# Optimization experiments

Measured on AMD Instinct MI355X. Metric: run time of the kernel, lower is better.

Reference implementation:

```python
import jax, jax.numpy as jnp
import numpy as np

D_MODEL = 256

def setup_inputs() -> dict:
    key = jax.random.key(0)
    k1, k2, k3, k4, k5, k6 = jax.random.split(key, 6)
    B, LQ, LK, D = 16, 2048, 2048, D_MODEL
    q = jax.random.normal(k1, (B, LQ, D), dtype=jnp.float32)
    k = jax.random.normal(k2, (B, LK, D), dtype=jnp.float32)
    tsp = jax.random.normal(k3, (B, LK, D), dtype=jnp.float32)
    # xavier_uniform for w_qk [D, D] (no bias)
    bound = float(np.sqrt(6.0 / (D + D)))
    w_qk = jax.random.uniform(k4, (D, D), minval=-bound, maxval=bound, dtype=jnp.float32)
    # linear1: default torch init kaiming-uniform-ish; any values fine for correctness baseline
    lim = float(1.0 / np.sqrt(D))
    w1 = jax.random.uniform(k5, (D, D), minval=-lim, maxval=lim, dtype=jnp.float32)
    b1 = jax.random.uniform(k6, (D,), minval=-lim, maxval=lim, dtype=jnp.float32)
    return {"q": q, "k": k, "tsp": tsp, "w_qk": w_qk, "w1": w1, "b1": b1}

def reference(q, k, tsp, w_qk, w1, b1):
    d_head = q.shape[-1]
    temperature = jnp.asarray(np.power(d_head, 0.5), dtype=q.dtype)
    residual = q
    # shared Q/K projection (torch Linear: x @ W^T)
    qp = jnp.einsum('bqd,ed->bqe', q, w_qk)            # [B, Lq, Dh]
    kp = jnp.einsum('bkd,ed->bke', k, w_qk)            # [B, Lk, Dh]
    logits = jnp.einsum('bqd,bkd->bqk', qp, kp) / temperature  # [B, Lq, Lk]
    attn = jax.nn.softmax(logits, axis=2)
    # sigmoid is monotonic: max(sigmoid(x)) == sigmoid(max(x))
    prob_fg = jax.nn.sigmoid(jnp.max(logits, axis=-1, keepdims=True))  # [B, Lq, 1]
    out = jnp.einsum('bqk,bkd->bqd', attn, tsp)        # [B, Lq, Dh]
    gated = (residual + out) * prob_fg
    return jnp.einsum('bqd,ed->bqe', gated, w1) + b1
```

## Files before the change

kernel.cpp:

```cpp
#include <hip/hip_runtime.h>
#include <hip/hip_bf16.h>

typedef __bf16 bf16;
typedef __bf16 bf16x8 __attribute__((ext_vector_type(8)));
typedef __bf16 bf16x4 __attribute__((ext_vector_type(4)));
typedef __bf16 bf16x2 __attribute__((ext_vector_type(2)));
typedef float f32x4 __attribute__((ext_vector_type(4)));

static __device__ __forceinline__ f32x4 mfma16(bf16x8 a, bf16x8 b, f32x4 c) {
    return __builtin_amdgcn_mfma_f32_16x16x32_bf16(a, b, c, 0, 0, 0);
}

static __device__ __forceinline__ void load16_to_lds(const void* g, void* l) {
    __builtin_amdgcn_global_load_lds(
        (const __attribute__((address_space(1))) unsigned int*)g,
        (__attribute__((address_space(3))) unsigned int*)l, 16, 0, 0);
}

#define LKV 2048
#define DM 256

template<bool IN_BF16, bool OUT_BF16, bool HAS_BIAS>
static __device__ __forceinline__ void gemm_body(char* smem,
                                                 const void* __restrict__ Xv,
                                                 const float* __restrict__ Wf,
                                                 const float* __restrict__ bias,
                                                 float scale, void* __restrict__ Y,
                                                 long rowbase) {
    bf16* Xl  = (bf16*)smem;
    char* WlB = smem + 33792;
    const int tid  = threadIdx.x;
    const int lane = tid & 63, wave = tid >> 6;
    const int hi = lane >> 4, lo = lane & 15;

    if (IN_BF16) {
        const bf16* Xb = (const bf16*)Xv;
#pragma unroll
        for (int i = 0; i < 8; ++i) {
            int idx = i * 256 + tid;
            int r = idx >> 5, c8 = (idx & 31) * 8;
            uint4 v = *(const uint4*)(Xb + (rowbase + r) * 256 + c8);
            *(uint4*)(Xl + r * 264 + c8) = v;
        }
    } else {
        const float* X = (const float*)Xv;
#pragma unroll
        for (int i = 0; i < 16; ++i) {
            int idx4 = i * 256 + tid;
            int e = idx4 * 4;
            int r = e >> 8, c = e & 255;
            float4 v = *(const float4*)(X + (rowbase + r) * 256 + c);
            bf16x4 o;
            o[0] = (bf16)v.x; o[1] = (bf16)v.y; o[2] = (bf16)v.z; o[3] = (bf16)v.w;
            *(bf16x4*)(Xl + r * 264 + c) = o;
        }
    }

    f32x4 acc[16];
    const f32x4 zero = {0.f, 0.f, 0.f, 0.f};
#pragma unroll
    for (int n = 0; n < 16; ++n) acc[n] = zero;

    for (int ks = 0; ks < 8; ++ks) {
        __syncthreads();
#pragma unroll
        for (int c = 0; c < 8; ++c) {
            int idx = c * 256 + tid;
            int e = idx >> 3, q4 = (idx & 7) * 4;
            float4 v = *(const float4*)(Wf + e * 256 + ks * 32 + q4);
            bf16x4 o;
            o[0] = (bf16)v.x; o[1] = (bf16)v.y; o[2] = (bf16)v.z; o[3] = (bf16)v.w;
            *(bf16x4*)(WlB + e * 80 + q4 * 2) = o;
        }
        __syncthreads();
        bf16x8 a = *(const bf16x8*)((const char*)Xl + (wave * 16 + lo) * 528 + ks * 64 + hi * 16);
#pragma unroll
        for (int n = 0; n < 16; ++n) {
            bf16x8 bfr = *(const bf16x8*)(WlB + (n * 16 + lo) * 80 + hi * 16);
            acc[n] = mfma16(a, bfr, acc[n]);
        }
    }

#pragma unroll
    for (int n = 0; n < 16; ++n) {
        int col = n * 16 + lo;
        float bv = HAS_BIAS ? bias[col] : 0.f;
#pragma unroll
        for (int r = 0; r < 4; ++r) {
            long row = rowbase + wave * 16 + hi * 4 + r;
            float v = acc[n][r] * scale + bv;
            if (OUT_BF16) ((bf16*)Y)[row * 256 + col] = (bf16)v;
            else          ((float*)Y)[row * 256 + col] = v;
        }
    }
}

__global__ __launch_bounds__(256) void prep_qk(const float* __restrict__ q,
                                               const float* __restrict__ k,
                                               const float* __restrict__ wqk,
                                               const float* __restrict__ tsp,
                                               bf16* __restrict__ qp,
                                               bf16* __restrict__ kp,
                                               bf16* __restrict__ tspF) {
    __shared__ __align__(16) char smem[54272];
    const int tid = threadIdx.x;
    int bid = (int)blockIdx.x;
    if (bid < 1024) {
        bool is_k = bid >= 512;
        gemm_body<false, true, false>(smem, is_k ? k : q, wqk, nullptr,
                                      is_k ? 1.0f : 0.0625f, is_k ? kp : qp,
                                      (long)(bid & 511) * 64);
        return;
    }
    int id = bid - 1024;
    const int b = id >> 7;
    const int kv0 = (id & 31) * 64, d0 = ((id >> 5) & 3) * 64;
    float (*tile)[65] = (float(*)[65])smem;
#pragma unroll
    for (int i = 0; i < 4; ++i) {
        int idx = i * 256 + tid;
        int kv = idx >> 4, c4 = (idx & 15) * 4;
        float4 v = *(const float4*)(tsp + ((long)(b * LKV + kv0 + kv)) * DM + d0 + c4);
        tile[kv][c4 + 0] = v.x; tile[kv][c4 + 1] = v.y;
        tile[kv][c4 + 2] = v.z; tile[kv][c4 + 3] = v.w;
    }
    __syncthreads();
    char* outb = (char*)tspF + ((long)b << 20);
#pragma unroll
    for (int i = 0; i < 2; ++i) {
        int w = i * 256 + tid;
        int ti = w >> 8;
        int dti = (w >> 6) & 3;
        int lane = w & 63;
        int hi = lane >> 4, lo = lane & 15;
        bf16x8 o;
#pragma unroll
        for (int j = 0; j < 8; ++j) o[j] = (bf16)tile[ti * 32 + hi * 8 + j][dti * 16 + lo];
        int t_abs = (kv0 >> 5) + ti;
        int dt_abs = (d0 >> 4) + dti;
        *(bf16x8*)(outb + (((t_abs * 16 + dt_abs) << 6) + lane) * 16) = o;
    }
}

__global__ __launch_bounds__(256) void gemm_out(const bf16* __restrict__ gated,
                                                const float* __restrict__ w1,
                                                const float* __restrict__ b1,
                                                float* __restrict__ out) {
    __shared__ __align__(16) char smem[54272];
    gemm_body<true, false, true>(smem, gated, w1, b1, 1.0f, out, (long)blockIdx.x * 64);
}

__global__ __launch_bounds__(256, 2) void flash6(const bf16* __restrict__ qp,
                                                 const bf16* __restrict__ kp,
                                                 const bf16* __restrict__ tspF,
                                                 const float* __restrict__ qorig,
                                                 bf16* __restrict__ gated) {
    __shared__ __align__(16) char kbuf[3][16384];
    const int tid  = threadIdx.x;
    const int lane = tid & 63, wave = tid >> 6;
    const int hi = lane >> 4, lo = lane & 15;

    int id  = (int)blockIdx.x;
    int bid = (id & 7) * 64 + (id >> 3);
    const int b  = bid >> 5;
    const int qb = bid & 31;
    const long qbase = (long)b * LKV + qb * 64;
    const char* kp_g  = (const char*)(kp + (long)b * LKV * DM);
    const char* tsp_f = (const char*)tspF + ((long)b << 20) + lane * 16;

    int kp_off[4];
#pragma unroll
    for (int j = 0; j < 4; ++j) {
        int kv = wave * 8 + j * 2 + (lane >> 5);
        kp_off[j] = kv * 512 + (((lane & 31) ^ (kv & 7)) << 4);
    }

    int bp_src[4];
#pragma unroll
    for (int k2 = 0; k2 < 4; ++k2)
        bp_src[k2] = ((((hi & 1) * 2 + (k2 >> 1)) << 4) + lo) << 2;

    bf16x8 aq[8];
    {
        const bf16* qrow = qp + (qbase + wave * 16 + lo) * DM;
#pragma unroll
        for (int ks = 0; ks < 8; ++ks) aq[ks] = *(const bf16x8*)(qrow + ks * 32 + hi * 8);
    }

    bf16x8 ones;
#pragma unroll
    for (int j = 0; j < 8; ++j) ones[j] = (bf16)1.0f;

    f32x4 o[16], o_l;
    const f32x4 zero = {0.f, 0.f, 0.f, 0.f};
#pragma unroll
    for (int n = 0; n < 16; ++n) o[n] = zero;
    o_l = zero;
    float m = -1e30f, tm = -1e30f;

    const int kswz = (lo & 7) << 4;

#pragma unroll
    for (int j = 0; j < 4; ++j)
        load16_to_lds(kp_g + kp_off[j],          &kbuf[0][wave * 4096 + j * 1024]);
#pragma unroll
    for (int j = 0; j < 4; ++j)
        load16_to_lds(kp_g + 16384 + kp_off[j],  &kbuf[1][wave * 4096 + j * 1024]);

    for (int t = 0; t < 64; ++t) {
        if (t == 0)       { asm volatile("s_waitcnt vmcnt(4)"  ::: "memory"); }
        else if (t == 63) { asm volatile("s_waitcnt vmcnt(16)" ::: "memory"); }
        else              { asm volatile("s_waitcnt vmcnt(20)" ::: "memory"); }
        __builtin_amdgcn_sched_barrier(0);
        __builtin_amdgcn_s_barrier();
        __builtin_amdgcn_sched_barrier(0);

        bf16x8 tt[16];
        {
            const char* tb = tsp_f + (long)t * 16384;
#pragma unroll
            for (int dt = 0; dt < 16; ++dt)
                tt[dt] = *(const bf16x8*)(tb + dt * 1024);
        }
        if (t < 62) {
            const int dslot = (t + 2) % 3;
            const char* src = kp_g + (long)(t + 2) * 16384;
#pragma unroll
            for (int j = 0; j < 4; ++j)
                load16_to_lds(src + kp_off[j], &kbuf[dslot][wave * 4096 + j * 1024]);
        }
        __builtin_amdgcn_sched_barrier(0);

        f32x4 s[2];
        const char* kb = kbuf[t % 3];
        __builtin_amdgcn_s_setprio(1);
#pragma unroll
        for (int n = 0; n < 2; ++n) {
            s[n] = zero;
            const char* rowp = kb + ((n * 16 + lo) << 9);
#pragma unroll
            for (int ks = 0; ks < 8; ++ks) {
                bf16x8 kk = *(const bf16x8*)(rowp + ((ks * 64 + hi * 16) ^ kswz));
                s[n] = mfma16(kk, aq[ks], s[n]);
            }
        }
        __builtin_amdgcn_s_setprio(0);

        float pm = fmaxf(fmaxf(fmaxf(s[0][0], s[0][1]), fmaxf(s[0][2], s[0][3])),
                         fmaxf(fmaxf(s[1][0], s[1][1]), fmaxf(s[1][2], s[1][3])));
        pm = fmaxf(pm, __shfl_xor(pm, 16));
        pm = fmaxf(pm, __shfl_xor(pm, 32));
        tm = fmaxf(tm, pm);
        if (__any(pm > m + 8.f)) {
            float nm = fmaxf(m, pm);
            float a = __expf(m - nm);
            m = nm;
            o_l *= a;
#pragma unroll
            for (int n = 0; n < 16; ++n) o[n] *= a;
        }
        int cvt[2][2];
#pragma unroll
        for (int n = 0; n < 2; ++n)
#pragma unroll
            for (int c = 0; c < 2; ++c) {
                bf16x2 pr;
                pr[0] = (bf16)__expf(s[n][2 * c]     - m);
                pr[1] = (bf16)__expf(s[n][2 * c + 1] - m);
                cvt[n][c] = __builtin_bit_cast(int, pr);
            }
        int pki[4];
#pragma unroll
        for (int k2 = 0; k2 < 4; ++k2) {
            int a0 = __builtin_amdgcn_ds_bpermute(bp_src[k2], cvt[0][k2 & 1]);
            int a1 = __builtin_amdgcn_ds_bpermute(bp_src[k2], cvt[1][k2 & 1]);
            pki[k2] = (hi < 2) ? a0 : a1;
        }
        int4 pii = make_int4(pki[0], pki[1], pki[2], pki[3]);
        bf16x8 pk = __builtin_bit_cast(bf16x8, pii);

        o_l = mfma16(ones, pk, o_l);
        __builtin_amdgcn_s_setprio(1);
#pragma unroll
        for (int dt = 0; dt < 16; ++dt)
            o[dt] = mfma16(tt[dt], pk, o[dt]);
        __builtin_amdgcn_s_setprio(0);
    }

    float prob = 1.f / (1.f + __expf(-tm));
    float invl = 1.f / o_l[0];
    long row = qbase + wave * 16 + lo;
#pragma unroll
    for (int dt = 0; dt < 16; ++dt) {
        int c0 = dt * 16 + hi * 4;
        float4 qv = *(const float4*)(qorig + row * 256 + c0);
        bf16x4 g;
        g[0] = (bf16)((qv.x + o[dt][0] * invl) * prob);
        g[1] = (bf16)((qv.y + o[dt][1] * invl) * prob);
        g[2] = (bf16)((qv.z + o[dt][2] * invl) * prob);
        g[3] = (bf16)((qv.w + o[dt][3] * invl) * prob);
        *(bf16x4*)(gated + row * 256 + c0) = g;
    }
}

extern "C" void kernel_launch(void* const* d_in, const int* in_sizes, int n_in,
                              void* d_out, int out_size, void* d_ws, size_t ws_size,
                              hipStream_t stream) {
    const float* q    = (const float*)d_in[0];
    const float* k    = (const float*)d_in[1];
    const float* tsp  = (const float*)d_in[2];
    const float* w_qk = (const float*)d_in[3];
    const float* w1   = (const float*)d_in[4];
    const float* b1   = (const float*)d_in[5];
    float* out = (float*)d_out;
    char* ws = (char*)d_ws;

    bf16* qp_b  = (bf16*)(ws + 0);
    bf16* kp_b  = (bf16*)(ws + 16777216);
    bf16* tspF  = (bf16*)(ws + 33554432);
    bf16* gated = (bf16*)(ws + 50331648);

    prep_qk<<<3072, 256, 0, stream>>>(q, k, w_qk, tsp, qp_b, kp_b, tspF);

    flash6<<<512, 256, 0, stream>>>(qp_b, kp_b, tspF, q, gated);

    gemm_out<<<512, 256, 0, stream>>>(gated, w1, b1, out);
}
```

Measured before the change: 182.4 us.

## Process two query groups per wave and software-pipeline QK with PV across iterations

The flash kernel now handles 128 query rows per block (32 per wave, in two 16-row groups), so each K tile from LDS and each tsp fragment from global memory is reused for two MFMA groups. The loop is manually pipelined: the PV MFMAs for the previous tile are issued alongside the QK MFMAs of the current tile, with double-buffered tsp registers. Softmax switches to exp2 by folding log2(e) into the Q scale, with a larger rescale threshold and a compensating ln2 factor in the sigmoid gate. The cost is roughly double the register pressure, occupancy reduced to one block per CU, and a grid of 256 blocks.

```diff
diff --git a/kernel.cpp b/kernel.cpp
--- a/kernel.cpp
+++ b/kernel.cpp
@@ -108,7 +108,7 @@
     if (bid < 1024) {
         bool is_k = bid >= 512;
         gemm_body<false, true, false>(smem, is_k ? k : q, wqk, nullptr,
-                                      is_k ? 1.0f : 0.0625f, is_k ? kp : qp,
+                                      is_k ? 1.0f : 0.09016844f, is_k ? kp : qp,
                                       (long)(bid & 511) * 64);
         return;
     }
@@ -150,21 +150,21 @@
     gemm_body<true, false, true>(smem, gated, w1, b1, 1.0f, out, (long)blockIdx.x * 64);
 }
 
-__global__ __launch_bounds__(256, 2) void flash6(const bf16* __restrict__ qp,
+__global__ __launch_bounds__(256, 1) void flash7(const bf16* __restrict__ qp,
                                                  const bf16* __restrict__ kp,
                                                  const bf16* __restrict__ tspF,
                                                  const float* __restrict__ qorig,
                                                  bf16* __restrict__ gated) {
-    __shared__ __align__(16) char kbuf[3][16384];
+    __shared__ __align__(16) char kbuf[3 * 16384];
     const int tid  = threadIdx.x;
     const int lane = tid & 63, wave = tid >> 6;
     const int hi = lane >> 4, lo = lane & 15;
 
     int id  = (int)blockIdx.x;
-    int bid = (id & 7) * 64 + (id >> 3);
-    const int b  = bid >> 5;
-    const int qb = bid & 31;
-    const long qbase = (long)b * LKV + qb * 64;
+    int bid = (id & 7) * 32 + (id >> 3);
+    const int b  = bid >> 4;
+    const int qb = bid & 15;
+    const long qbase = (long)b * LKV + qb * 128;
     const char* kp_g  = (const char*)(kp + (long)b * LKV * DM);
     const char* tsp_f = (const char*)tspF + ((long)b << 20) + lane * 16;
 
@@ -174,133 +174,173 @@
         int kv = wave * 8 + j * 2 + (lane >> 5);
         kp_off[j] = kv * 512 + (((lane & 31) ^ (kv & 7)) << 4);
     }
-
     int bp_src[4];
 #pragma unroll
     for (int k2 = 0; k2 < 4; ++k2)
         bp_src[k2] = ((((hi & 1) * 2 + (k2 >> 1)) << 4) + lo) << 2;
 
-    bf16x8 aq[8];
+    bf16x8 aq[2][8];
+#pragma unroll
+    for (int g = 0; g < 2; ++g) {
+        const bf16* qrow = qp + (qbase + wave * 32 + g * 16 + lo) * DM;
+#pragma unroll
+        for (int ks = 0; ks < 8; ++ks) aq[g][ks] = *(const bf16x8*)(qrow + ks * 32 + hi * 8);
+    }
+
+    bf16x8 ones;
+#pragma unroll
+    for (int j = 0; j < 8; ++j) ones[j] = (bf16)1.0f;
+
+    f32x4 o[2][16], o_l[2];
+    const f32x4 zero = {0.f, 0.f, 0.f, 0.f};
+#pragma unroll
+    for (int g = 0; g < 2; ++g) { for (int n = 0; n < 16; ++n) o[g][n] = zero; o_l[g] = zero; }
+    float m[2] = {-1e30f, -1e30f}, tm[2] = {-1e30f, -1e30f};
+    bf16x8 pk[2];
+    bf16x8 tt0[16], tt1[16];
+
+    const int kswz = (lo & 7) << 4;
+
+#pragma unroll
+    for (int j = 0; j < 4; ++j)
+        load16_to_lds(kp_g + kp_off[j],          kbuf + wave * 4096 + j * 1024);
+#pragma unroll
+    for (int j = 0; j < 4; ++j)
+        load16_to_lds(kp_g + 16384 + kp_off[j],  kbuf + 16384 + wave * 4096 + j * 1024);
+
+#define SOFTMAX_PK()                                                              \
+    {                                                                             \
+        float pm[2];                                                              \
+        _Pragma("unroll")                                                         \
+        for (int g = 0; g < 2; ++g) {                                             \
+            float v = fmaxf(fmaxf(fmaxf(s[g][0][0], s[g][0][1]),                  \
+                                  fmaxf(s[g][0][2], s[g][0][3])),                 \
+                            fmaxf(fmaxf(s[g][1][0], s[g][1][1]),                  \
+                                  fmaxf(s[g][1][2], s[g][1][3])));                \
+            v = fmaxf(v, __shfl_xor(v, 16));                                      \
+            v = fmaxf(v, __shfl_xor(v, 32));                                      \
+            pm[g] = v;                                                            \
+            tm[g] = fmaxf(tm[g], v);                                              \
+        }                                                                         \
+        bool need = (pm[0] > m[0] + 11.5f) || (pm[1] > m[1] + 11.5f);             \
+        if (__any(need)) {                                                        \
+            _Pragma("unroll")                                                     \
+            for (int g = 0; g < 2; ++g) {                                         \
+                float nm = fmaxf(m[g], pm[g]);                                    \
+                float a = exp2f(m[g] - nm);                                       \
+                m[g] = nm;                                                        \
+                o_l[g] *= a;                                                      \
+                _Pragma("unroll")                                                 \
+                for (int n = 0; n < 16; ++n) o[g][n] *= a;                        \
+            }                                                                     \
+        }                                                                         \
+        _Pragma("unroll")                                                         \
+        for (int g = 0; g < 2; ++g) {                                             \
+            int cvt[2][2];                                                        \
+            _Pragma("unroll")                                                     \
+            for (int n = 0; n < 2; ++n)                                           \
+                _Pragma("unroll")                                                 \
+                for (int c = 0; c < 2; ++c) {                                     \
+                    bf16x2 pr;                                                    \
+                    pr[0] = (bf16)exp2f(s[g][n][2 * c]     - m[g]);               \
+                    pr[1] = (bf16)exp2f(s[g][n][2 * c + 1] - m[g]);               \
+                    cvt[n][c] = __builtin_bit_cast(int, pr);                      \
+                }                                                                 \
+            int pki[4];                                                           \
+            _Pragma("unroll")                                                     \
+            for (int k2 = 0; k2 < 4; ++k2) {                                      \
+                int a0 = __builtin_amdgcn_ds_bpermute(bp_src[k2], cvt[0][k2 & 1]);\
+                int a1 = __builtin_amdgcn_ds_bpermute(bp_src[k2], cvt[1][k2 & 1]);\
+                pki[k2] = (hi < 2) ? a0 : a1;                                     \
+            }                                                                     \
+            int4 pii = make_int4(pki[0], pki[1], pki[2], pki[3]);                 \
+            pk[g] = __builtin_bit_cast(bf16x8, pii);                              \
+        }                                                                         \
+    }
+
+#define PHASE(T, VMN, TTN, TTO, DO_PV, DO_DMA)                                    \
+    {                                                                             \
+        asm volatile("s_waitcnt vmcnt(" #VMN ")" ::: "memory");                   \
+        __builtin_amdgcn_sched_barrier(0);                                        \
+        __builtin_amdgcn_s_barrier();                                             \
+        __builtin_amdgcn_sched_barrier(0);                                        \
+        {                                                                         \
+            const char* tb = tsp_f + (long)(T) * 16384;                           \
+            _Pragma("unroll")                                                     \
+            for (int dt = 0; dt < 16; ++dt)                                       \
+                TTN[dt] = *(const bf16x8*)(tb + dt * 1024);                       \
+        }                                                                         \
+        if (DO_DMA) {                                                             \
+            const char* src = kp_g + (long)((T) + 2) * 16384;                     \
+            char* dst = kbuf + (((T) + 2) % 3) * 16384 + wave * 4096;             \
+            _Pragma("unroll")                                                     \
+            for (int j = 0; j < 4; ++j)                                           \
+                load16_to_lds(src + kp_off[j], dst + j * 1024);                   \
+        }                                                                         \
+        f32x4 s[2][2];                                                            \
+        s[0][0] = zero; s[0][1] = zero; s[1][0] = zero; s[1][1] = zero;           \
+        {                                                                         \
+            const char* kb = kbuf + ((T) % 3) * 16384;                            \
+            __builtin_amdgcn_s_setprio(1);                                        \
+            _Pragma("unroll")                                                     \
+            for (int n = 0; n < 2; ++n) {                                         \
+                const char* rowp = kb + ((n * 16 + lo) << 9);                     \
+                _Pragma("unroll")                                                 \
+                for (int ks = 0; ks < 8; ++ks) {                                  \
+                    bf16x8 kk = *(const bf16x8*)(rowp + ((ks * 64 + hi * 16) ^ kswz)); \
+                    s[0][n] = mfma16(kk, aq[0][ks], s[0][n]);                     \
+                    s[1][n] = mfma16(kk, aq[1][ks], s[1][n]);                     \
+                }                                                                 \
+            }                                                                     \
+            if (DO_PV) {                                                          \
+                o_l[0] = mfma16(ones, pk[0], o_l[0]);                             \
+                o_l[1] = mfma16(ones, pk[1], o_l[1]);                             \
+                _Pragma("unroll")                                                 \
+                for (int dt = 0; dt < 16; ++dt) {                                 \
+                    o[0][dt] = mfma16(TTO[dt], pk[0], o[0][dt]);                  \
+                    o[1][dt] = mfma16(TTO[dt], pk[1], o[1][dt]);                  \
+                }                                                                 \
+            }                                                                     \
+            __builtin_amdgcn_s_setprio(0);                                        \
+        }                                                                         \
+        SOFTMAX_PK();                                                             \
+    }
+
+    PHASE(0, 8, tt0, tt1, false, true)
+    for (int t = 1; t < 63; t += 2) {
+        PHASE(t,     24, tt1, tt0, true, (t     < 62))
+        PHASE(t + 1, 24, tt0, tt1, true, (t + 1 < 62))
+    }
+    PHASE(63, 16, tt1, tt0, true, false)
     {
-        const bf16* qrow = qp + (qbase + wave * 16 + lo) * DM;
-#pragma unroll
-        for (int ks = 0; ks < 8; ++ks) aq[ks] = *(const bf16x8*)(qrow + ks * 32 + hi * 8);
-    }
-
-    bf16x8 ones;
-#pragma unroll
-    for (int j = 0; j < 8; ++j) ones[j] = (bf16)1.0f;
-
-    f32x4 o[16], o_l;
-    const f32x4 zero = {0.f, 0.f, 0.f, 0.f};
-#pragma unroll
-    for (int n = 0; n < 16; ++n) o[n] = zero;
-    o_l = zero;
-    float m = -1e30f, tm = -1e30f;
-
-    const int kswz = (lo & 7) << 4;
-
-#pragma unroll
-    for (int j = 0; j < 4; ++j)
-        load16_to_lds(kp_g + kp_off[j],          &kbuf[0][wave * 4096 + j * 1024]);
-#pragma unroll
-    for (int j = 0; j < 4; ++j)
-        load16_to_lds(kp_g + 16384 + kp_off[j],  &kbuf[1][wave * 4096 + j * 1024]);
-
-    for (int t = 0; t < 64; ++t) {
-        if (t == 0)       { asm volatile("s_waitcnt vmcnt(4)"  ::: "memory"); }
-        else if (t == 63) { asm volatile("s_waitcnt vmcnt(16)" ::: "memory"); }
-        else              { asm volatile("s_waitcnt vmcnt(20)" ::: "memory"); }
-        __builtin_amdgcn_sched_barrier(0);
-        __builtin_amdgcn_s_barrier();
-        __builtin_amdgcn_sched_barrier(0);
-
-        bf16x8 tt[16];
-        {
-            const char* tb = tsp_f + (long)t * 16384;
-#pragma unroll
-            for (int dt = 0; dt < 16; ++dt)
-                tt[dt] = *(const bf16x8*)(tb + dt * 1024);
-        }
-        if (t < 62) {
-            const int dslot = (t + 2) % 3;
-            const char* src = kp_g + (long)(t + 2) * 16384;
-#pragma unroll
-            for (int j = 0; j < 4; ++j)
-                load16_to_lds(src + kp_off[j], &kbuf[dslot][wave * 4096 + j * 1024]);
-        }
-        __builtin_amdgcn_sched_barrier(0);
-
-        f32x4 s[2];
-        const char* kb = kbuf[t % 3];
-        __builtin_amdgcn_s_setprio(1);
-#pragma unroll
-        for (int n = 0; n < 2; ++n) {
-            s[n] = zero;
-            const char* rowp = kb + ((n * 16 + lo) << 9);
-#pragma unroll
-            for (int ks = 0; ks < 8; ++ks) {
-                bf16x8 kk = *(const bf16x8*)(rowp + ((ks * 64 + hi * 16) ^ kswz));
-                s[n] = mfma16(kk, aq[ks], s[n]);
-            }
-        }
-        __builtin_amdgcn_s_setprio(0);
-
-        float pm = fmaxf(fmaxf(fmaxf(s[0][0], s[0][1]), fmaxf(s[0][2], s[0][3])),
-                         fmaxf(fmaxf(s[1][0], s[1][1]), fmaxf(s[1][2], s[1][3])));
-        pm = fmaxf(pm, __shfl_xor(pm, 16));
-        pm = fmaxf(pm, __shfl_xor(pm, 32));
-        tm = fmaxf(tm, pm);
-        if (__any(pm > m + 8.f)) {
-            float nm = fmaxf(m, pm);
-            float a = __expf(m - nm);
-            m = nm;
-            o_l *= a;
-#pragma unroll
-            for (int n = 0; n < 16; ++n) o[n] *= a;
-        }
-        int cvt[2][2];
-#pragma unroll
-        for (int n = 0; n < 2; ++n)
-#pragma unroll
-            for (int c = 0; c < 2; ++c) {
-                bf16x2 pr;
-                pr[0] = (bf16)__expf(s[n][2 * c]     - m);
-                pr[1] = (bf16)__expf(s[n][2 * c + 1] - m);
-                cvt[n][c] = __builtin_bit_cast(int, pr);
-            }
-        int pki[4];
-#pragma unroll
-        for (int k2 = 0; k2 < 4; ++k2) {
-            int a0 = __builtin_amdgcn_ds_bpermute(bp_src[k2], cvt[0][k2 & 1]);
-            int a1 = __builtin_amdgcn_ds_bpermute(bp_src[k2], cvt[1][k2 & 1]);
-            pki[k2] = (hi < 2) ? a0 : a1;
-        }
-        int4 pii = make_int4(pki[0], pki[1], pki[2], pki[3]);
-        bf16x8 pk = __builtin_bit_cast(bf16x8, pii);
-
-        o_l = mfma16(ones, pk, o_l);
-        __builtin_amdgcn_s_setprio(1);
-#pragma unroll
-        for (int dt = 0; dt < 16; ++dt)
-            o[dt] = mfma16(tt[dt], pk, o[dt]);
-        __builtin_amdgcn_s_setprio(0);
-    }
-
-    float prob = 1.f / (1.f + __expf(-tm));
-    float invl = 1.f / o_l[0];
-    long row = qbase + wave * 16 + lo;
-#pragma unroll
-    for (int dt = 0; dt < 16; ++dt) {
-        int c0 = dt * 16 + hi * 4;
-        float4 qv = *(const float4*)(qorig + row * 256 + c0);
-        bf16x4 g;
-        g[0] = (bf16)((qv.x + o[dt][0] * invl) * prob);
-        g[1] = (bf16)((qv.y + o[dt][1] * invl) * prob);
-        g[2] = (bf16)((qv.z + o[dt][2] * invl) * prob);
-        g[3] = (bf16)((qv.w + o[dt][3] * invl) * prob);
-        *(bf16x4*)(gated + row * 256 + c0) = g;
-    }
+        o_l[0] = mfma16(ones, pk[0], o_l[0]);
+        o_l[1] = mfma16(ones, pk[1], o_l[1]);
+#pragma unroll
+        for (int dt = 0; dt < 16; ++dt) {
+            o[0][dt] = mfma16(tt1[dt], pk[0], o[0][dt]);
+            o[1][dt] = mfma16(tt1[dt], pk[1], o[1][dt]);
+        }
+    }
+
+#pragma unroll
+    for (int g = 0; g < 2; ++g) {
+        float prob = 1.f / (1.f + __expf(-tm[g] * 0.69314718f));
+        float invl = 1.f / o_l[g][0];
+        long row = qbase + wave * 32 + g * 16 + lo;
+#pragma unroll
+        for (int dt = 0; dt < 16; ++dt) {
+            int c0 = dt * 16 + hi * 4;
+            float4 qv = *(const float4*)(qorig + row * 256 + c0);
+            bf16x4 gg;
+            gg[0] = (bf16)((qv.x + o[g][dt][0] * invl) * prob);
+            gg[1] = (bf16)((qv.y + o[g][dt][1] * invl) * prob);
+            gg[2] = (bf16)((qv.z + o[g][dt][2] * invl) * prob);
+            gg[3] = (bf16)((qv.w + o[g][dt][3] * invl) * prob);
+            *(bf16x4*)(gated + row * 256 + c0) = gg;
+        }
+    }
+#undef PHASE
+#undef SOFTMAX_PK
 }
 
 extern "C" void kernel_launch(void* const* d_in, const int* in_sizes, int n_in,
@@ -322,7 +362,7 @@
 
     prep_qk<<<3072, 256, 0, stream>>>(q, k, w_qk, tsp, qp_b, kp_b, tspF);
 
-    flash6<<<512, 256, 0, stream>>>(qp_b, kp_b, tspF, q, gated);
+    flash7<<<256, 256, 0, stream>>>(qp_b, kp_b, tspF, q, gated);
 
     gemm_out<<<512, 256, 0, stream>>>(gated, w1, b1, out);
 }
```

Measured after the change: 202.1 us. 10.8% more time.

## Rewrite flash kernel with 32x32 MFMA, split-KV halves, and exp2 softmax

Applied to the files above, without the earlier changes.

The attention kernel now uses 512-thread blocks covering 128 query rows. Two wave groups each process half of the KV sequence and merge their partial softmax states and outputs through LDS at the end. Score and PV products switch to 32x32x16 MFMA tiles, and the Q scale folds in log2(e) so exp2 can be used. The key LDS buffer drops from triple to double buffering, and tsp fragments are loaded incrementally in registers. This trades higher register pressure and an extra barrier per iteration, plus the merge epilogue, for fewer instructions and more work per wave.

```diff
diff --git a/kernel.cpp b/kernel.cpp
--- a/kernel.cpp
+++ b/kernel.cpp
@@ -6,9 +6,13 @@
 typedef __bf16 bf16x4 __attribute__((ext_vector_type(4)));
 typedef __bf16 bf16x2 __attribute__((ext_vector_type(2)));
 typedef float f32x4 __attribute__((ext_vector_type(4)));
+typedef float f32x16 __attribute__((ext_vector_type(16)));
 
 static __device__ __forceinline__ f32x4 mfma16(bf16x8 a, bf16x8 b, f32x4 c) {
     return __builtin_amdgcn_mfma_f32_16x16x32_bf16(a, b, c, 0, 0, 0);
+}
+static __device__ __forceinline__ f32x16 mfma32(bf16x8 a, bf16x8 b, f32x16 c) {
+    return __builtin_amdgcn_mfma_f32_32x32x16_bf16(a, b, c, 0, 0, 0);
 }
 
 static __device__ __forceinline__ void load16_to_lds(const void* g, void* l) {
@@ -108,7 +112,7 @@
     if (bid < 1024) {
         bool is_k = bid >= 512;
         gemm_body<false, true, false>(smem, is_k ? k : q, wqk, nullptr,
-                                      is_k ? 1.0f : 0.0625f, is_k ? kp : qp,
+                                      is_k ? 1.0f : 0.09016844f, is_k ? kp : qp,
                                       (long)(bid & 511) * 64);
         return;
     }
@@ -131,14 +135,14 @@
         int w = i * 256 + tid;
         int ti = w >> 8;
         int dti = (w >> 6) & 3;
-        int lane = w & 63;
-        int hi = lane >> 4, lo = lane & 15;
+        int fl = w & 63;
+        int hi = fl >> 4, lo = fl & 15;
         bf16x8 o;
 #pragma unroll
         for (int j = 0; j < 8; ++j) o[j] = (bf16)tile[ti * 32 + hi * 8 + j][dti * 16 + lo];
         int t_abs = (kv0 >> 5) + ti;
         int dt_abs = (d0 >> 4) + dti;
-        *(bf16x8*)(outb + (((t_abs * 16 + dt_abs) << 6) + lane) * 16) = o;
+        *(bf16x8*)(outb + (((t_abs * 16 + dt_abs) << 6) + fl) * 16) = o;
     }
 }
 
@@ -150,156 +154,197 @@
     gemm_body<true, false, true>(smem, gated, w1, b1, 1.0f, out, (long)blockIdx.x * 64);
 }
 
-__global__ __launch_bounds__(256, 2) void flash6(const bf16* __restrict__ qp,
+__global__ __launch_bounds__(512, 2) void flash9(const bf16* __restrict__ qp,
                                                  const bf16* __restrict__ kp,
                                                  const bf16* __restrict__ tspF,
                                                  const float* __restrict__ qorig,
                                                  bf16* __restrict__ gated) {
-    __shared__ __align__(16) char kbuf[3][16384];
+    __shared__ __align__(16) char smem[67072];
     const int tid  = threadIdx.x;
     const int lane = tid & 63, wave = tid >> 6;
-    const int hi = lane >> 4, lo = lane & 15;
+    const int half = wave >> 2, w4 = wave & 3;
+    const int l31 = lane & 31, hi32 = lane >> 5;
 
     int id  = (int)blockIdx.x;
-    int bid = (id & 7) * 64 + (id >> 3);
-    const int b  = bid >> 5;
-    const int qb = bid & 31;
-    const long qbase = (long)b * LKV + qb * 64;
-    const char* kp_g  = (const char*)(kp + (long)b * LKV * DM);
-    const char* tsp_f = (const char*)tspF + ((long)b << 20) + lane * 16;
+    int bid = (id & 7) * 32 + (id >> 3);
+    const int b  = bid >> 4;
+    const int qb = bid & 15;
+    const long qbase = (long)b * LKV + qb * 128;
+    const char* kp_g  = (const char*)(kp + (long)b * LKV * DM) + half * 524288;
+    const char* tsp_f = (const char*)tspF + ((long)b << 20);
+    char* kbase = smem + half * 32768;
 
     int kp_off[4];
 #pragma unroll
     for (int j = 0; j < 4; ++j) {
-        int kv = wave * 8 + j * 2 + (lane >> 5);
+        int kv = w4 * 8 + j * 2 + (lane >> 5);
         kp_off[j] = kv * 512 + (((lane & 31) ^ (kv & 7)) << 4);
     }
-
-    int bp_src[4];
-#pragma unroll
-    for (int k2 = 0; k2 < 4; ++k2)
-        bp_src[k2] = ((((hi & 1) * 2 + (k2 >> 1)) << 4) + lo) << 2;
-
-    bf16x8 aq[8];
+    const int kswz = (l31 & 7) << 4;
+    const int tfo0 = ((l31 >> 4) << 10) + ((l31 & 15) << 4) + (hi32 << 8);
+
+    bf16x8 aq[16];
     {
-        const bf16* qrow = qp + (qbase + wave * 16 + lo) * DM;
-#pragma unroll
-        for (int ks = 0; ks < 8; ++ks) aq[ks] = *(const bf16x8*)(qrow + ks * 32 + hi * 8);
-    }
-
-    bf16x8 ones;
-#pragma unroll
-    for (int j = 0; j < 8; ++j) ones[j] = (bf16)1.0f;
-
-    f32x4 o[16], o_l;
-    const f32x4 zero = {0.f, 0.f, 0.f, 0.f};
-#pragma unroll
-    for (int n = 0; n < 16; ++n) o[n] = zero;
-    o_l = zero;
-    float m = -1e30f, tm = -1e30f;
-
-    const int kswz = (lo & 7) << 4;
+        const bf16* qrow = qp + (qbase + w4 * 32 + l31) * DM;
+#pragma unroll
+        for (int ki = 0; ki < 16; ++ki)
+            aq[ki] = *(const bf16x8*)(qrow + ki * 16 + hi32 * 8);
+    }
+
+    const f32x16 z16 = {0.f,0.f,0.f,0.f,0.f,0.f,0.f,0.f,0.f,0.f,0.f,0.f,0.f,0.f,0.f,0.f};
+    f32x16 o[8];
+#pragma unroll
+    for (int n = 0; n < 8; ++n) o[n] = z16;
+    float l_own = 0.f, m = -1e30f, tm = -1e30f;
 
 #pragma unroll
     for (int j = 0; j < 4; ++j)
-        load16_to_lds(kp_g + kp_off[j],          &kbuf[0][wave * 4096 + j * 1024]);
+        load16_to_lds(kp_g + kp_off[j],          kbase + w4 * 4096 + j * 1024);
 #pragma unroll
     for (int j = 0; j < 4; ++j)
-        load16_to_lds(kp_g + 16384 + kp_off[j],  &kbuf[1][wave * 4096 + j * 1024]);
-
-    for (int t = 0; t < 64; ++t) {
-        if (t == 0)       { asm volatile("s_waitcnt vmcnt(4)"  ::: "memory"); }
-        else if (t == 63) { asm volatile("s_waitcnt vmcnt(16)" ::: "memory"); }
-        else              { asm volatile("s_waitcnt vmcnt(20)" ::: "memory"); }
+        load16_to_lds(kp_g + 16384 + kp_off[j],  kbase + 16384 + w4 * 4096 + j * 1024);
+
+    for (int t = 0; t < 32; ++t) {
+        if (t < 31) { asm volatile("s_waitcnt vmcnt(4)" ::: "memory"); }
+        else        { asm volatile("s_waitcnt vmcnt(0)" ::: "memory"); }
         __builtin_amdgcn_sched_barrier(0);
         __builtin_amdgcn_s_barrier();
         __builtin_amdgcn_sched_barrier(0);
 
-        bf16x8 tt[16];
-        {
-            const char* tb = tsp_f + (long)t * 16384;
-#pragma unroll
-            for (int dt = 0; dt < 16; ++dt)
-                tt[dt] = *(const bf16x8*)(tb + dt * 1024);
-        }
-        if (t < 62) {
-            const int dslot = (t + 2) % 3;
-            const char* src = kp_g + (long)(t + 2) * 16384;
-#pragma unroll
-            for (int j = 0; j < 4; ++j)
-                load16_to_lds(src + kp_off[j], &kbuf[dslot][wave * 4096 + j * 1024]);
-        }
+        const char* ttb = tsp_f + (long)(half * 32 + t) * 16384;
+        bf16x8 tt[3][2];
+        tt[0][0] = *(const bf16x8*)(ttb + tfo0);
+        tt[0][1] = *(const bf16x8*)(ttb + tfo0 + 512);
+        tt[1][0] = *(const bf16x8*)(ttb + 2048 + tfo0);
+        tt[1][1] = *(const bf16x8*)(ttb + 2048 + tfo0 + 512);
+
+        f32x16 s = z16;
+        const char* kb = kbase + (t & 1) * 16384;
+        __builtin_amdgcn_s_setprio(1);
+#pragma unroll
+        for (int ki = 0; ki < 16; ++ki) {
+            bf16x8 kk = *(const bf16x8*)(kb + l31 * 512 + ((ki * 32 + hi32 * 16) ^ kswz));
+            s = mfma32(kk, aq[ki], s);
+        }
+        __builtin_amdgcn_s_setprio(0);
+
         __builtin_amdgcn_sched_barrier(0);
-
-        f32x4 s[2];
-        const char* kb = kbuf[t % 3];
-        __builtin_amdgcn_s_setprio(1);
-#pragma unroll
-        for (int n = 0; n < 2; ++n) {
-            s[n] = zero;
-            const char* rowp = kb + ((n * 16 + lo) << 9);
-#pragma unroll
-            for (int ks = 0; ks < 8; ++ks) {
-                bf16x8 kk = *(const bf16x8*)(rowp + ((ks * 64 + hi * 16) ^ kswz));
-                s[n] = mfma16(kk, aq[ks], s[n]);
-            }
-        }
-        __builtin_amdgcn_s_setprio(0);
-
-        float pm = fmaxf(fmaxf(fmaxf(s[0][0], s[0][1]), fmaxf(s[0][2], s[0][3])),
-                         fmaxf(fmaxf(s[1][0], s[1][1]), fmaxf(s[1][2], s[1][3])));
-        pm = fmaxf(pm, __shfl_xor(pm, 16));
+        __builtin_amdgcn_s_barrier();
+        __builtin_amdgcn_sched_barrier(0);
+
+        float pm = s[0];
+#pragma unroll
+        for (int r = 1; r < 16; ++r) pm = fmaxf(pm, s[r]);
         pm = fmaxf(pm, __shfl_xor(pm, 32));
         tm = fmaxf(tm, pm);
-        if (__any(pm > m + 8.f)) {
+        if (__any(pm > m + 11.5f)) {
             float nm = fmaxf(m, pm);
-            float a = __expf(m - nm);
+            float a = exp2f(m - nm);
             m = nm;
-            o_l *= a;
-#pragma unroll
-            for (int n = 0; n < 16; ++n) o[n] *= a;
-        }
-        int cvt[2][2];
-#pragma unroll
-        for (int n = 0; n < 2; ++n)
-#pragma unroll
-            for (int c = 0; c < 2; ++c) {
-                bf16x2 pr;
-                pr[0] = (bf16)__expf(s[n][2 * c]     - m);
-                pr[1] = (bf16)__expf(s[n][2 * c + 1] - m);
-                cvt[n][c] = __builtin_bit_cast(int, pr);
+            l_own *= a;
+#pragma unroll
+            for (int n = 0; n < 8; ++n) o[n] *= a;
+        }
+        float p[16];
+        float ls = 0.f;
+#pragma unroll
+        for (int r = 0; r < 16; ++r) { p[r] = exp2f(s[r] - m); ls += p[r]; }
+        l_own += ls;
+
+        int w[8];
+#pragma unroll
+        for (int i = 0; i < 8; ++i) {
+            bf16x2 pr; pr[0] = (bf16)p[2 * i]; pr[1] = (bf16)p[2 * i + 1];
+            w[i] = __builtin_bit_cast(int, pr);
+        }
+        int x0 = __shfl_xor(w[0], 32), x1 = __shfl_xor(w[1], 32);
+        int x2 = __shfl_xor(w[2], 32), x3 = __shfl_xor(w[3], 32);
+        int x4 = __shfl_xor(w[4], 32), x5 = __shfl_xor(w[5], 32);
+        int x6 = __shfl_xor(w[6], 32), x7 = __shfl_xor(w[7], 32);
+        int4 f0i, f1i;
+        if (hi32 == 0) { f0i = make_int4(w[0], w[1], x0, x1); f1i = make_int4(w[4], w[5], x4, x5); }
+        else           { f0i = make_int4(x2, x3, w[2], w[3]); f1i = make_int4(x6, x7, w[6], w[7]); }
+        bf16x8 pf0 = __builtin_bit_cast(bf16x8, f0i);
+        bf16x8 pf1 = __builtin_bit_cast(bf16x8, f1i);
+
+        __builtin_amdgcn_s_setprio(1);
+#pragma unroll
+        for (int db = 0; db < 8; ++db) {
+            if (db < 6) {
+                const char* t2 = ttb + (db + 2) * 2048;
+                tt[(db + 2) % 3][0] = *(const bf16x8*)(t2 + tfo0);
+                tt[(db + 2) % 3][1] = *(const bf16x8*)(t2 + tfo0 + 512);
             }
-        int pki[4];
-#pragma unroll
-        for (int k2 = 0; k2 < 4; ++k2) {
-            int a0 = __builtin_amdgcn_ds_bpermute(bp_src[k2], cvt[0][k2 & 1]);
-            int a1 = __builtin_amdgcn_ds_bpermute(bp_src[k2], cvt[1][k2 & 1]);
-            pki[k2] = (hi < 2) ? a0 : a1;
-        }
-        int4 pii = make_int4(pki[0], pki[1], pki[2], pki[3]);
-        bf16x8 pk = __builtin_bit_cast(bf16x8, pii);
-
-        o_l = mfma16(ones, pk, o_l);
-        __builtin_amdgcn_s_setprio(1);
-#pragma unroll
-        for (int dt = 0; dt < 16; ++dt)
-            o[dt] = mfma16(tt[dt], pk, o[dt]);
+            o[db] = mfma32(tt[db % 3][0], pf0, o[db]);
+            o[db] = mfma32(tt[db % 3][1], pf1, o[db]);
+        }
         __builtin_amdgcn_s_setprio(0);
-    }
-
-    float prob = 1.f / (1.f + __expf(-tm));
-    float invl = 1.f / o_l[0];
-    long row = qbase + wave * 16 + lo;
-#pragma unroll
-    for (int dt = 0; dt < 16; ++dt) {
-        int c0 = dt * 16 + hi * 4;
-        float4 qv = *(const float4*)(qorig + row * 256 + c0);
-        bf16x4 g;
-        g[0] = (bf16)((qv.x + o[dt][0] * invl) * prob);
-        g[1] = (bf16)((qv.y + o[dt][1] * invl) * prob);
-        g[2] = (bf16)((qv.z + o[dt][2] * invl) * prob);
-        g[3] = (bf16)((qv.w + o[dt][3] * invl) * prob);
-        *(bf16x4*)(gated + row * 256 + c0) = g;
+
+        if (t < 30) {
+            const char* src = kp_g + (long)(t + 2) * 16384;
+            char* dst = kbase + (t & 1) * 16384 + w4 * 4096;
+#pragma unroll
+            for (int j = 0; j < 4; ++j)
+                load16_to_lds(src + kp_off[j], dst + j * 1024);
+        }
+    }
+
+    __syncthreads();
+    float l2 = l_own + __shfl_xor(l_own, 32);
+    float* lmt = (float*)(smem + 65536);
+    if (half == 1 && hi32 == 0) {
+        int qi = w4 * 32 + l31;
+        lmt[qi * 3 + 0] = l2; lmt[qi * 3 + 1] = m; lmt[qi * 3 + 2] = tm;
+    }
+    float aA = 1.f, aB = 0.f, invl = 0.f, prob = 0.f;
+    long row = qbase + w4 * 32 + l31;
+#pragma unroll
+    for (int round = 0; round < 2; ++round) {
+        __syncthreads();
+        if (half == 1) {
+#pragma unroll
+            for (int db = 0; db < 4; ++db) {
+                float* dst = (float*)smem + (w4 * 4 + db) * 1024 + lane * 16;
+                f32x16 v = o[round * 4 + db];
+#pragma unroll
+                for (int c = 0; c < 4; ++c) {
+                    float4 f4;
+                    f4.x = v[c * 4 + 0]; f4.y = v[c * 4 + 1];
+                    f4.z = v[c * 4 + 2]; f4.w = v[c * 4 + 3];
+                    *(float4*)(dst + c * 4) = f4;
+                }
+            }
+        }
+        __syncthreads();
+        if (half == 0) {
+            if (round == 0) {
+                int qi = w4 * 32 + l31;
+                float lB = lmt[qi * 3 + 0], mB = lmt[qi * 3 + 1], tmB = lmt[qi * 3 + 2];
+                float M = fmaxf(m, mB);
+                aA = exp2f(m - M); aB = exp2f(mB - M);
+                invl = 1.f / (l2 * aA + lB * aB);
+                float tmM = fmaxf(tm, tmB);
+                prob = 1.f / (1.f + __expf(-tmM * 0.69314718f));
+            }
+#pragma unroll
+            for (int db = 0; db < 4; ++db) {
+                const float* srcp = (const float*)smem + (w4 * 4 + db) * 1024 + lane * 16;
+                f32x16 oc = o[round * 4 + db];
+                int d0 = (round * 4 + db) * 32;
+#pragma unroll
+                for (int g2 = 0; g2 < 4; ++g2) {
+                    float4 ob = *(const float4*)(srcp + g2 * 4);
+                    int d = d0 + g2 * 8 + hi32 * 4;
+                    float4 qv = *(const float4*)(qorig + row * 256 + d);
+                    bf16x4 gg;
+                    gg[0] = (bf16)((qv.x + (oc[g2 * 4 + 0] * aA + ob.x * aB) * invl) * prob);
+                    gg[1] = (bf16)((qv.y + (oc[g2 * 4 + 1] * aA + ob.y * aB) * invl) * prob);
+                    gg[2] = (bf16)((qv.z + (oc[g2 * 4 + 2] * aA + ob.z * aB) * invl) * prob);
+                    gg[3] = (bf16)((qv.w + (oc[g2 * 4 + 3] * aA + ob.w * aB) * invl) * prob);
+                    *(bf16x4*)(gated + row * 256 + d) = gg;
+                }
+            }
+        }
     }
 }
 
@@ -322,7 +367,7 @@
 
     prep_qk<<<3072, 256, 0, stream>>>(q, k, w_qk, tsp, qp_b, kp_b, tspF);
 
-    flash6<<<512, 256, 0, stream>>>(qp_b, kp_b, tspF, q, gated);
+    flash9<<<256, 512, 0, stream>>>(qp_b, kp_b, tspF, q, gated);
 
     gemm_out<<<512, 256, 0, stream>>>(gated, w1, b1, out);
 }
```

After: 270.6 us. 1.48x slower.

## Split KV sequence across two blocks and merge partials in output GEMM

Applied to the files above, without the earlier changes.

The attention kernel now splits the 2048-key range into two halves handled by separate blocks (1024 blocks, occupancy hint 4). Each half writes unnormalised bf16 partial outputs plus row sum, max and true max, and the output GEMM kernel merges the two halves, applies residual and sigmoid gate, then multiplies by w1. Other changes: the Q scale folds in log2(e) so exp2f replaces expf, the row sum is accumulated in scalar registers instead of via an MFMA with a ones vector, and the K buffer drops from triple to double buffering with Q fragments and tsp loads streamed per iteration. This adds extra global traffic for the partial outputs and leaves less prefetch slack.

```diff
diff --git a/kernel.cpp b/kernel.cpp
--- a/kernel.cpp
+++ b/kernel.cpp
@@ -108,7 +108,7 @@
     if (bid < 1024) {
         bool is_k = bid >= 512;
         gemm_body<false, true, false>(smem, is_k ? k : q, wqk, nullptr,
-                                      is_k ? 1.0f : 0.0625f, is_k ? kp : qp,
+                                      is_k ? 1.0f : 0.09016844f, is_k ? kp : qp,
                                       (long)(bid & 511) * 64);
         return;
     }
@@ -131,42 +131,36 @@
         int w = i * 256 + tid;
         int ti = w >> 8;
         int dti = (w >> 6) & 3;
-        int lane = w & 63;
-        int hi = lane >> 4, lo = lane & 15;
+        int fl = w & 63;
+        int hi = fl >> 4, lo = fl & 15;
         bf16x8 o;
 #pragma unroll
         for (int j = 0; j < 8; ++j) o[j] = (bf16)tile[ti * 32 + hi * 8 + j][dti * 16 + lo];
         int t_abs = (kv0 >> 5) + ti;
         int dt_abs = (d0 >> 4) + dti;
-        *(bf16x8*)(outb + (((t_abs * 16 + dt_abs) << 6) + lane) * 16) = o;
-    }
-}
-
-__global__ __launch_bounds__(256) void gemm_out(const bf16* __restrict__ gated,
-                                                const float* __restrict__ w1,
-                                                const float* __restrict__ b1,
-                                                float* __restrict__ out) {
-    __shared__ __align__(16) char smem[54272];
-    gemm_body<true, false, true>(smem, gated, w1, b1, 1.0f, out, (long)blockIdx.x * 64);
-}
-
-__global__ __launch_bounds__(256, 2) void flash6(const bf16* __restrict__ qp,
-                                                 const bf16* __restrict__ kp,
-                                                 const bf16* __restrict__ tspF,
-                                                 const float* __restrict__ qorig,
-                                                 bf16* __restrict__ gated) {
-    __shared__ __align__(16) char kbuf[3][16384];
+        *(bf16x8*)(outb + (((t_abs * 16 + dt_abs) << 6) + fl) * 16) = o;
+    }
+}
+
+__global__ __launch_bounds__(256, 4) void flash10(const bf16* __restrict__ qp,
+                                                  const bf16* __restrict__ kp,
+                                                  const bf16* __restrict__ tspF,
+                                                  bf16* __restrict__ oPart,
+                                                  float* __restrict__ lmt) {
+    __shared__ __align__(16) char kbuf[2][16384];
     const int tid  = threadIdx.x;
     const int lane = tid & 63, wave = tid >> 6;
     const int hi = lane >> 4, lo = lane & 15;
 
     int id  = (int)blockIdx.x;
-    int bid = (id & 7) * 64 + (id >> 3);
-    const int b  = bid >> 5;
-    const int qb = bid & 31;
-    const long qbase = (long)b * LKV + qb * 64;
-    const char* kp_g  = (const char*)(kp + (long)b * LKV * DM);
-    const char* tsp_f = (const char*)tspF + ((long)b << 20) + lane * 16;
+    int bid = (id & 7) * 128 + (id >> 3);
+    const int b    = bid >> 6;
+    const int qb   = (bid >> 1) & 31;
+    const int half = bid & 1;
+    const long qbase  = (long)b * LKV + qb * 64;
+    const char* kp_g  = (const char*)(kp + (long)b * LKV * DM) + half * 524288;
+    const char* tsp_f = (const char*)tspF + ((long)b << 20) + (long)half * 524288 + lane * 16;
+    const bf16* qrow  = qp + (qbase + wave * 16 + lo) * DM;
 
     int kp_off[4];
 #pragma unroll
@@ -174,101 +168,76 @@
         int kv = wave * 8 + j * 2 + (lane >> 5);
         kp_off[j] = kv * 512 + (((lane & 31) ^ (kv & 7)) << 4);
     }
-
     int bp_src[4];
 #pragma unroll
     for (int k2 = 0; k2 < 4; ++k2)
         bp_src[k2] = ((((hi & 1) * 2 + (k2 >> 1)) << 4) + lo) << 2;
-
-    bf16x8 aq[8];
-    {
-        const bf16* qrow = qp + (qbase + wave * 16 + lo) * DM;
-#pragma unroll
-        for (int ks = 0; ks < 8; ++ks) aq[ks] = *(const bf16x8*)(qrow + ks * 32 + hi * 8);
-    }
-
-    bf16x8 ones;
-#pragma unroll
-    for (int j = 0; j < 8; ++j) ones[j] = (bf16)1.0f;
-
-    f32x4 o[16], o_l;
+    const int kswz = (lo & 7) << 4;
+
+    f32x4 o[16];
     const f32x4 zero = {0.f, 0.f, 0.f, 0.f};
 #pragma unroll
     for (int n = 0; n < 16; ++n) o[n] = zero;
-    o_l = zero;
-    float m = -1e30f, tm = -1e30f;
-
-    const int kswz = (lo & 7) << 4;
+    float m = -1e30f, tm = -1e30f, l = 0.f;
 
 #pragma unroll
     for (int j = 0; j < 4; ++j)
-        load16_to_lds(kp_g + kp_off[j],          &kbuf[0][wave * 4096 + j * 1024]);
-#pragma unroll
-    for (int j = 0; j < 4; ++j)
-        load16_to_lds(kp_g + 16384 + kp_off[j],  &kbuf[1][wave * 4096 + j * 1024]);
-
-    for (int t = 0; t < 64; ++t) {
-        if (t == 0)       { asm volatile("s_waitcnt vmcnt(4)"  ::: "memory"); }
-        else if (t == 63) { asm volatile("s_waitcnt vmcnt(16)" ::: "memory"); }
-        else              { asm volatile("s_waitcnt vmcnt(20)" ::: "memory"); }
+        load16_to_lds(kp_g + kp_off[j], &kbuf[0][wave * 4096 + j * 1024]);
+
+    for (int t = 0; t < 32; ++t) {
+        asm volatile("s_waitcnt vmcnt(0)" ::: "memory");
         __builtin_amdgcn_sched_barrier(0);
         __builtin_amdgcn_s_barrier();
         __builtin_amdgcn_sched_barrier(0);
 
-        bf16x8 tt[16];
-        {
-            const char* tb = tsp_f + (long)t * 16384;
-#pragma unroll
-            for (int dt = 0; dt < 16; ++dt)
-                tt[dt] = *(const bf16x8*)(tb + dt * 1024);
-        }
-        if (t < 62) {
-            const int dslot = (t + 2) % 3;
-            const char* src = kp_g + (long)(t + 2) * 16384;
+        if (t < 31) {
+            const char* src = kp_g + (long)(t + 1) * 16384;
+            char* dst = &kbuf[(t + 1) & 1][wave * 4096];
 #pragma unroll
             for (int j = 0; j < 4; ++j)
-                load16_to_lds(src + kp_off[j], &kbuf[dslot][wave * 4096 + j * 1024]);
-        }
-        __builtin_amdgcn_sched_barrier(0);
-
-        f32x4 s[2];
-        const char* kb = kbuf[t % 3];
+                load16_to_lds(src + kp_off[j], dst + j * 1024);
+        }
+
+        f32x4 s0 = zero, s1 = zero;
+        const char* kb = kbuf[t & 1];
         __builtin_amdgcn_s_setprio(1);
 #pragma unroll
-        for (int n = 0; n < 2; ++n) {
-            s[n] = zero;
-            const char* rowp = kb + ((n * 16 + lo) << 9);
-#pragma unroll
-            for (int ks = 0; ks < 8; ++ks) {
-                bf16x8 kk = *(const bf16x8*)(rowp + ((ks * 64 + hi * 16) ^ kswz));
-                s[n] = mfma16(kk, aq[ks], s[n]);
-            }
+        for (int ks = 0; ks < 8; ++ks) {
+            bf16x8 aqv = *(const bf16x8*)(qrow + ks * 32 + hi * 8);
+            bf16x8 k0 = *(const bf16x8*)(kb + (lo << 9) + ((ks * 64 + hi * 16) ^ kswz));
+            bf16x8 k1 = *(const bf16x8*)(kb + ((16 + lo) << 9) + ((ks * 64 + hi * 16) ^ kswz));
+            s0 = mfma16(k0, aqv, s0);
+            s1 = mfma16(k1, aqv, s1);
         }
         __builtin_amdgcn_s_setprio(0);
 
-        float pm = fmaxf(fmaxf(fmaxf(s[0][0], s[0][1]), fmaxf(s[0][2], s[0][3])),
-                         fmaxf(fmaxf(s[1][0], s[1][1]), fmaxf(s[1][2], s[1][3])));
+        float pm = fmaxf(fmaxf(fmaxf(s0[0], s0[1]), fmaxf(s0[2], s0[3])),
+                         fmaxf(fmaxf(s1[0], s1[1]), fmaxf(s1[2], s1[3])));
         pm = fmaxf(pm, __shfl_xor(pm, 16));
         pm = fmaxf(pm, __shfl_xor(pm, 32));
         tm = fmaxf(tm, pm);
-        if (__any(pm > m + 8.f)) {
+        if (__any(pm > m + 11.5f)) {
             float nm = fmaxf(m, pm);
-            float a = __expf(m - nm);
+            float a = exp2f(m - nm);
             m = nm;
-            o_l *= a;
+            l *= a;
 #pragma unroll
             for (int n = 0; n < 16; ++n) o[n] *= a;
         }
+        float p00 = exp2f(s0[0] - m), p01 = exp2f(s0[1] - m);
+        float p02 = exp2f(s0[2] - m), p03 = exp2f(s0[3] - m);
+        float p10 = exp2f(s1[0] - m), p11 = exp2f(s1[1] - m);
+        float p12 = exp2f(s1[2] - m), p13 = exp2f(s1[3] - m);
+        l += (p00 + p01) + (p02 + p03) + (p10 + p11) + (p12 + p13);
+
         int cvt[2][2];
-#pragma unroll
-        for (int n = 0; n < 2; ++n)
-#pragma unroll
-            for (int c = 0; c < 2; ++c) {
-                bf16x2 pr;
-                pr[0] = (bf16)__expf(s[n][2 * c]     - m);
-                pr[1] = (bf16)__expf(s[n][2 * c + 1] - m);
-                cvt[n][c] = __builtin_bit_cast(int, pr);
-            }
+        {
+            bf16x2 pr;
+            pr[0] = (bf16)p00; pr[1] = (bf16)p01; cvt[0][0] = __builtin_bit_cast(int, pr);
+            pr[0] = (bf16)p02; pr[1] = (bf16)p03; cvt[0][1] = __builtin_bit_cast(int, pr);
+            pr[0] = (bf16)p10; pr[1] = (bf16)p11; cvt[1][0] = __builtin_bit_cast(int, pr);
+            pr[0] = (bf16)p12; pr[1] = (bf16)p13; cvt[1][1] = __builtin_bit_cast(int, pr);
+        }
         int pki[4];
 #pragma unroll
         for (int k2 = 0; k2 < 4; ++k2) {
@@ -279,27 +248,121 @@
         int4 pii = make_int4(pki[0], pki[1], pki[2], pki[3]);
         bf16x8 pk = __builtin_bit_cast(bf16x8, pii);
 
-        o_l = mfma16(ones, pk, o_l);
+        const char* ttb = tsp_f + (long)t * 16384;
+        bf16x8 w[4];
+#pragma unroll
+        for (int i = 0; i < 4; ++i) w[i] = *(const bf16x8*)(ttb + i * 1024);
         __builtin_amdgcn_s_setprio(1);
 #pragma unroll
-        for (int dt = 0; dt < 16; ++dt)
-            o[dt] = mfma16(tt[dt], pk, o[dt]);
+        for (int dt = 0; dt < 16; ++dt) {
+            o[dt] = mfma16(w[dt & 3], pk, o[dt]);
+            if (dt < 12) w[dt & 3] = *(const bf16x8*)(ttb + (dt + 4) * 1024);
+        }
         __builtin_amdgcn_s_setprio(0);
     }
 
-    float prob = 1.f / (1.f + __expf(-tm));
-    float invl = 1.f / o_l[0];
-    long row = qbase + wave * 16 + lo;
+    l += __shfl_xor(l, 16);
+    l += __shfl_xor(l, 32);
+    long orow = ((((long)b * 32 + qb) * 2 + half) * 64 + wave * 16 + lo) * 256;
 #pragma unroll
     for (int dt = 0; dt < 16; ++dt) {
-        int c0 = dt * 16 + hi * 4;
-        float4 qv = *(const float4*)(qorig + row * 256 + c0);
+        bf16x4 ov;
+        ov[0] = (bf16)o[dt][0]; ov[1] = (bf16)o[dt][1];
+        ov[2] = (bf16)o[dt][2]; ov[3] = (bf16)o[dt][3];
+        *(bf16x4*)(oPart + orow + dt * 16 + hi * 4) = ov;
+    }
+    if (hi == 0) {
+        long li = ((((long)b * 32 + qb) * 2 + half) * 64 + wave * 16 + lo) * 4;
+        lmt[li + 0] = l; lmt[li + 1] = m; lmt[li + 2] = tm;
+    }
+}
+
+__global__ __launch_bounds__(256) void gemm_out_merge(const float* __restrict__ qg,
+                                                      const bf16* __restrict__ oPart,
+                                                      const float* __restrict__ lmt,
+                                                      const float* __restrict__ w1,
+                                                      const float* __restrict__ b1,
+                                                      float* __restrict__ out) {
+    __shared__ __align__(16) char smem[55296];
+    bf16* Xl   = (bf16*)smem;
+    char* WlB  = smem + 33792;
+    float* sRow = (float*)(smem + 54272);
+    const int tid  = threadIdx.x;
+    const int lane = tid & 63, wave = tid >> 6;
+    const int hi = lane >> 4, lo = lane & 15;
+    const long rowbase = (long)blockIdx.x * 64;
+    const int b  = (int)(rowbase >> 11);
+    const int qb = (int)(rowbase >> 6) & 31;
+    const long obase = (((long)b * 32 + qb) * 2) * 16384;
+    const int lbase  = ((b * 32 + qb) * 2) * 64;
+
+    if (tid < 64) {
+        float lA = lmt[(lbase + tid) * 4 + 0];
+        float mA = lmt[(lbase + tid) * 4 + 1];
+        float tA = lmt[(lbase + tid) * 4 + 2];
+        float lB = lmt[(lbase + 64 + tid) * 4 + 0];
+        float mB = lmt[(lbase + 64 + tid) * 4 + 1];
+        float tB = lmt[(lbase + 64 + tid) * 4 + 2];
+        float M  = fmaxf(mA, mB);
+        float aA = exp2f(mA - M), aB = exp2f(mB - M);
+        float invl = 1.f / (lA * aA + lB * aB);
+        sRow[tid * 4 + 0] = aA * invl;
+        sRow[tid * 4 + 1] = aB * invl;
+        sRow[tid * 4 + 2] = 1.f / (1.f + __expf(-fmaxf(tA, tB) * 0.69314718f));
+    }
+    __syncthreads();
+
+#pragma unroll
+    for (int i = 0; i < 16; ++i) {
+        int idx4 = i * 256 + tid;
+        int e = idx4 * 4;
+        int r = e >> 8, c = e & 255;
+        float4 qv = *(const float4*)(qg + (rowbase + r) * 256 + c);
+        bf16x4 oa = *(const bf16x4*)(oPart + obase + r * 256 + c);
+        bf16x4 ob = *(const bf16x4*)(oPart + obase + 16384 + r * 256 + c);
+        float f0 = sRow[r * 4 + 0], f1 = sRow[r * 4 + 1], pr = sRow[r * 4 + 2];
         bf16x4 g;
-        g[0] = (bf16)((qv.x + o[dt][0] * invl) * prob);
-        g[1] = (bf16)((qv.y + o[dt][1] * invl) * prob);
-        g[2] = (bf16)((qv.z + o[dt][2] * invl) * prob);
-        g[3] = (bf16)((qv.w + o[dt][3] * invl) * prob);
-        *(bf16x4*)(gated + row * 256 + c0) = g;
+        g[0] = (bf16)((qv.x + (float)oa[0] * f0 + (float)ob[0] * f1) * pr);
+        g[1] = (bf16)((qv.y + (float)oa[1] * f0 + (float)ob[1] * f1) * pr);
+        g[2] = (bf16)((qv.z + (float)oa[2] * f0 + (float)ob[2] * f1) * pr);
+        g[3] = (bf16)((qv.w + (float)oa[3] * f0 + (float)ob[3] * f1) * pr);
+        *(bf16x4*)(Xl + r * 264 + c) = g;
+    }
+
+    f32x4 acc[16];
+    const f32x4 zero = {0.f, 0.f, 0.f, 0.f};
+#pragma unroll
+    for (int n = 0; n < 16; ++n) acc[n] = zero;
+
+    for (int ks = 0; ks < 8; ++ks) {
+        __syncthreads();
+#pragma unroll
+        for (int c = 0; c < 8; ++c) {
+            int idx = c * 256 + tid;
+            int e = idx >> 3, q4 = (idx & 7) * 4;
+            float4 v = *(const float4*)(w1 + e * 256 + ks * 32 + q4);
+            bf16x4 o;
+            o[0] = (bf16)v.x; o[1] = (bf16)v.y; o[2] = (bf16)v.z; o[3] = (bf16)v.w;
+            *(bf16x4*)(WlB + e * 80 + q4 * 2) = o;
+        }
+        __syncthreads();
+        bf16x8 a = *(const bf16x8*)((const char*)Xl + (wave * 16 + lo) * 528 + ks * 64 + hi * 16);
+#pragma unroll
+        for (int n = 0; n < 16; ++n) {
+            bf16x8 bfr = *(const bf16x8*)(WlB + (n * 16 + lo) * 80 + hi * 16);
+            acc[n] = mfma16(a, bfr, acc[n]);
+        }
+    }
+
+#pragma unroll
+    for (int n = 0; n < 16; ++n) {
+        int col = n * 16 + lo;
+        float bv = b1[col];
+#pragma unroll
+        for (int r = 0; r < 4; ++r) {
+            long row = rowbase + wave * 16 + hi * 4 + r;
+            out[row * 256 + col] = acc[n][r] + bv;
+        }
     }
 }
 
@@ -315,14 +378,15 @@
     float* out = (float*)d_out;
     char* ws = (char*)d_ws;
 
-    bf16* qp_b  = (bf16*)(ws + 0);
-    bf16* kp_b  = (bf16*)(ws + 16777216);
-    bf16* tspF  = (bf16*)(ws + 33554432);
-    bf16* gated = (bf16*)(ws + 50331648);
+    bf16*  qp_b  = (bf16*)(ws + 0);
+    bf16*  kp_b  = (bf16*)(ws + 16777216);
+    bf16*  tspF  = (bf16*)(ws + 33554432);
+    bf16*  oPart = (bf16*)(ws + 50331648);
+    float* lmt   = (float*)(ws + 83886080);
 
     prep_qk<<<3072, 256, 0, stream>>>(q, k, w_qk, tsp, qp_b, kp_b, tspF);
 
-    flash6<<<512, 256, 0, stream>>>(qp_b, kp_b, tspF, q, gated);
-
-    gemm_out<<<512, 256, 0, stream>>>(gated, w1, b1, out);
-}
+    flash10<<<1024, 256, 0, stream>>>(qp_b, kp_b, tspF, oPart, lmt);
+
+    gemm_out_merge<<<512, 256, 0, stream>>>(q, oPart, lmt, w1, b1, out);
+}
```

Measured after the change: 332.0 us. 82.0% more time.
